# Performance work log

Hardware: AMD Instinct MI355X
Metric: run time of the kernel (lower is better)

Reference implementation:

```python
import jax, jax.numpy as jnp
import numpy as np

N = 4096          # nodes
F_IN = 1386       # txt_feat_len
NHID = 1024       # per-head hidden
NHEADS = 8
CODE = 64         # code_len
LRELU_ALPHA = 0.2
NEG_INF = -9e15


def _build_adj(x):
    # F.normalize + cosine sim, threshold 0.8, sign -> {0,1}, then symmetric D^-1/2 A D^-1/2
    norm = jnp.maximum(jnp.linalg.norm(x, axis=1, keepdims=True), 1e-12)
    xn = x / norm
    sim = xn @ xn.T                                  # (N,N)
    A = (sim >= 0.8).astype(x.dtype)                 # sign after thresholding
    rowsum = A.sum(axis=1)
    r = jnp.where(rowsum > 0, rowsum ** -0.5, 0.0)
    adj = r[:, None] * A * r[None, :]                # symmetric normalized
    return jax.lax.stop_gradient(adj)                # torch code detaches x / adj is non-diff


def _gat_head(x, W, a, adj, concat):
    # x: (N,Fin), W: (Fin,H), a: (2H,1)
    H = W.shape[1]
    Wh = x @ W                                        # (N,H)
    f1 = Wh @ a[:H]                                   # (N,1)
    f2 = Wh @ a[H:]                                   # (N,1)
    e = jax.nn.leaky_relu(f1 + f2.T, LRELU_ALPHA)     # (N,N) pairwise scores
    e = jnp.where(adj > 0, e, NEG_INF)
    att = jax.nn.softmax(e, axis=1)                   # masked softmax (dropout off: eval)
    h = att @ Wh                                      # (N,H)
    return jax.nn.elu(h) if concat else h


def setup_inputs() -> dict:
    key = jax.random.key(0)
    k = jax.random.split(key, 5)
    x = jax.random.normal(k[0], (N, F_IN), dtype=jnp.float32)
    s_in = 1.0 / np.sqrt(F_IN)
    W_att = jax.random.uniform(k[1], (NHEADS, F_IN, NHID), jnp.float32, -s_in, s_in)
    a_att = jax.random.uniform(k[2], (NHEADS, 2 * NHID, 1), jnp.float32, -0.1, 0.1)
    s_h = 1.0 / np.sqrt(NHEADS * NHID)
    W_out = jax.random.uniform(k[3], (NHEADS * NHID, CODE), jnp.float32, -s_h, s_h)
    a_out = jax.random.uniform(k[4], (2 * CODE, 1), jnp.float32, -0.1, 0.1)
    return {"x": x, "W_att": W_att, "a_att": a_att, "W_out": W_out, "a_out": a_out}


def reference(x, W_att, a_att, W_out, a_out):
    adj = _build_adj(x)
    # 8 concat heads, vmapped over the head axis
    heads = jax.vmap(lambda W, a: _gat_head(x, W, a, adj, True))(W_att, a_att)  # (8,N,NHID)
    h = jnp.transpose(heads, (1, 0, 2)).reshape(N, NHEADS * NHID)               # cat dim=1
    out = _gat_head(h, W_out, a_out, adj, False)                                # (N,CODE)
    code = jnp.tanh(1.0 * out)                                                   # alpha=1.0
    return code
```

## Files before the change

### kernel.cpp

```cpp
#include <hip/hip_runtime.h>
#include <hip/hip_bf16.h>
#include <stdint.h>
#include <math.h>


typedef __bf16 bf16x8 __attribute__((ext_vector_type(8)));
typedef float  f32x4  __attribute__((ext_vector_type(4)));
typedef int    i32x4  __attribute__((ext_vector_type(4)));
typedef unsigned short ushort8 __attribute__((ext_vector_type(8)));

#define AS1C(p) ((const __attribute__((address_space(1))) void*)(p))
#define AS3(p)  ((__attribute__((address_space(3))) void*)(p))

#define MODE_WH  0
#define MODE_F32 2

__device__ __forceinline__ float bfbits2f(unsigned short u) {
    return __uint_as_float(((unsigned)u) << 16);
}
__device__ __forceinline__ unsigned short f2bfbits(float v) {
    __hip_bfloat16 b = __float2bfloat16(v);
    return *(unsigned short*)&b;
}

__device__ __forceinline__ bool row_fast(const unsigned* __restrict__ mask,
                                         const unsigned* __restrict__ summ,
                                         int row)
{
    const uint4 s = *(const uint4*)(summ + row * 4);
    unsigned sw[4] = { s.x, s.y, s.z, s.w };
    const int wi = row >> 5;
    bool fast = (sw[wi >> 5] == (1u << (wi & 31)));
    sw[wi >> 5] = 0;
    fast = fast && !(sw[0] | sw[1] | sw[2] | sw[3]);
    return fast && (mask[row * 128 + wi] == (1u << (row & 31)));
}

template<int MODE>
__device__ __forceinline__ void gemm_body(
    __hip_bfloat16* __restrict__ As, __hip_bfloat16* __restrict__ Bs,
    int bx, int by,
    const __hip_bfloat16* __restrict__ A,
    const __hip_bfloat16* __restrict__ B,
    int lda, int ldb, int K,
    void* __restrict__ Cv, int ldc, int Nreal,
    unsigned* __restrict__ mask,
    unsigned* __restrict__ summary,
    __hip_bfloat16* __restrict__ hout)
{
    const int tid  = threadIdx.x;
    const int lane = tid & 63;
    const int wave = tid >> 6;
    const int m0   = bx * 128;
    const int n0   = by * 128;

    f32x4 acc[4][4];
#pragma unroll
    for (int i = 0; i < 4; ++i)
#pragma unroll
        for (int j = 0; j < 4; ++j)
#pragma unroll
            for (int k = 0; k < 4; ++k) acc[i][j][k] = 0.f;

    const int wm = wave >> 1, wn = wave & 1;
    const int q  = lane >> 4, ln = lane & 15;

    const int kIters = K >> 6;
    for (int kt = 0; kt < kIters; ++kt) {
        __syncthreads();
#pragma unroll
        for (int p = 0; p < 4; ++p) {
            const int t    = p * 256 + tid;
            const int half = t >> 9;
            const int tl   = t & 511;
            const int row  = tl >> 2;
            const int kb   = (tl & 3) ^ ((tl >> 3) & 3);
            const int kofs = kt * 64 + half * 32 + kb * 8;
            const __hip_bfloat16* ga = A + (long long)(m0 + row) * lda + kofs;
            const __hip_bfloat16* gb = B + (long long)(n0 + row) * ldb + kofs;
            __hip_bfloat16* sa = As + (p * 256 + wave * 64) * 8;
            __hip_bfloat16* sb = Bs + (p * 256 + wave * 64) * 8;
            __builtin_amdgcn_global_load_lds(AS1C(ga), AS3(sa), 16, 0, 0);
            __builtin_amdgcn_global_load_lds(AS1C(gb), AS3(sb), 16, 0, 0);
        }
        __syncthreads();

#pragma unroll
        for (int s = 0; s < 2; ++s) {
            bf16x8 afr[4], bfr[4];
#pragma unroll
            for (int rg = 0; rg < 4; ++rg) {
                const int r  = wm * 64 + rg * 16 + ln;
                const int sl = q ^ ((r >> 1) & 3);
                afr[rg] = *(const bf16x8*)(As + s * 4096 + r * 32 + sl * 8);
            }
#pragma unroll
            for (int cg = 0; cg < 4; ++cg) {
                const int r  = wn * 64 + cg * 16 + ln;
                const int sl = q ^ ((r >> 1) & 3);
                bfr[cg] = *(const bf16x8*)(Bs + s * 4096 + r * 32 + sl * 8);
            }
#pragma unroll
            for (int rg = 0; rg < 4; ++rg)
#pragma unroll
                for (int cg = 0; cg < 4; ++cg)
                    acc[rg][cg] = __builtin_amdgcn_mfma_f32_16x16x32_bf16(
                        afr[rg], bfr[cg], acc[rg][cg], 0, 0, 0);
        }
    }

#pragma unroll
    for (int rg = 0; rg < 4; ++rg) {
#pragma unroll
        for (int i = 0; i < 4; ++i) {
            const int row = m0 + wm * 64 + rg * 16 + q * 4 + i;
            bool fast = false;
            if (MODE == MODE_WH) fast = row_fast(mask, summary, row);
#pragma unroll
            for (int cg = 0; cg < 4; ++cg) {
                const int col = n0 + wn * 64 + cg * 16 + ln;
                const float v = acc[rg][cg][i];
                if (MODE == MODE_WH) {
                    if (fast) {
                        const float u = v > 0.f ? v : (__expf(v) - 1.f);
                        hout[(long long)row * 8192 + col] = __float2bfloat16(u);
                    } else {
                        __hip_bfloat16* C = (__hip_bfloat16*)Cv;
                        C[(long long)row * ldc + col] = __float2bfloat16(v);
                    }
                } else {
                    if (col < Nreal) {
                        float* C = (float*)Cv;
                        C[(long long)row * ldc + col] = v;
                    }
                }
            }
        }
    }
}

__device__ __forceinline__ void sim_i8_body(
    signed char* __restrict__ Aq, signed char* __restrict__ Bq,
    int bx, int by,
    const signed char* __restrict__ xq,
    const float* __restrict__ scales,
    const float* __restrict__ norms,
    unsigned* __restrict__ mask,
    unsigned* __restrict__ summary)
{
    const int tid  = threadIdx.x;
    const int lane = tid & 63;
    const int wave = tid >> 6;
    const int m0   = bx * 128;
    const int n0   = by * 128;

    i32x4 acc[4][4];
#pragma unroll
    for (int i = 0; i < 4; ++i)
#pragma unroll
        for (int j = 0; j < 4; ++j)
#pragma unroll
            for (int k = 0; k < 4; ++k) acc[i][j][k] = 0;

    const int wm = wave >> 1, wn = wave & 1;
    const int q  = lane >> 4, ln = lane & 15;

    for (int kt = 0; kt < 22; ++kt) {
        __syncthreads();
#pragma unroll
        for (int p = 0; p < 2; ++p) {
            const int t   = p * 256 + tid;
            const int row = t >> 2;
            const int kb  = (t & 3) ^ ((t >> 3) & 3);
            const signed char* ga = xq + (long long)(m0 + row) * 1408 + kt * 64 + kb * 16;
            const signed char* gb = xq + (long long)(n0 + row) * 1408 + kt * 64 + kb * 16;
            signed char* sa = Aq + (p * 256 + wave * 64) * 16;
            signed char* sb = Bq + (p * 256 + wave * 64) * 16;
            __builtin_amdgcn_global_load_lds(AS1C(ga), AS3(sa), 16, 0, 0);
            __builtin_amdgcn_global_load_lds(AS1C(gb), AS3(sb), 16, 0, 0);
        }
        __syncthreads();

        i32x4 afr[4], bfr[4];
#pragma unroll
        for (int rg = 0; rg < 4; ++rg) {
            const int r = wm * 64 + rg * 16 + ln;
            const int s = q ^ ((r >> 1) & 3);
            afr[rg] = *(const i32x4*)(Aq + r * 64 + s * 16);
        }
#pragma unroll
        for (int cg = 0; cg < 4; ++cg) {
            const int r = wn * 64 + cg * 16 + ln;
            const int s = q ^ ((r >> 1) & 3);
            bfr[cg] = *(const i32x4*)(Bq + r * 64 + s * 16);
        }
#pragma unroll
        for (int rg = 0; rg < 4; ++rg)
#pragma unroll
            for (int cg = 0; cg < 4; ++cg)
                acc[rg][cg] = __builtin_amdgcn_mfma_i32_16x16x64_i8(
                    afr[rg], bfr[cg], acc[rg][cg], 0, 0, 0);
    }

#pragma unroll
    for (int rg = 0; rg < 4; ++rg) {
#pragma unroll
        for (int i = 0; i < 4; ++i) {
            const int row = m0 + wm * 64 + rg * 16 + q * 4 + i;
            const float sr = scales[row], nr = norms[row];
#pragma unroll
            for (int cg = 0; cg < 4; ++cg) {
                const int col = n0 + wn * 64 + cg * 16 + ln;
                const float v = (float)acc[rg][cg][i] * (sr * scales[col]);
                if (v >= 0.8f * nr * norms[col]) {
                    atomicOr(&mask[row * 128 + (col >> 5)], 1u << (col & 31));
                    atomicOr(&summary[row * 4 + (col >> 10)], 1u << ((col >> 5) & 31));
                    atomicOr(&mask[col * 128 + (row >> 5)], 1u << (row & 31));
                    atomicOr(&summary[col * 4 + (row >> 10)], 1u << ((row >> 5) & 31));
                }
            }
        }
    }
}

__global__ __launch_bounds__(256)
void stage1(const float* __restrict__ x,
            const float* __restrict__ W_att,
            const float* __restrict__ W_out,
            const float* __restrict__ a_att,
            __hip_bfloat16* __restrict__ x_bf,
            signed char* __restrict__ xq,
            float* __restrict__ norms,
            float* __restrict__ scales,
            __hip_bfloat16* __restrict__ WoutT,
            float* __restrict__ wa,
            unsigned* __restrict__ mask,
            unsigned* __restrict__ summ)
{
    __shared__ float ts[32][33];
    __shared__ float red[4], redm[4], sh_s;
    const int id  = blockIdx.x;
    const int tid = threadIdx.x;

    if (id < 4096) {
        const int i = id;
        if (tid < 128) mask[i * 128 + tid] = 0;
        else if (tid < 132) summ[i * 4 + (tid - 128)] = 0;
        float ss = 0.f, am = 0.f;
        float vv[6];
#pragma unroll
        for (int k = 0; k < 6; ++k) {
            const int c = tid + k * 256;
            float v = (c < 1386) ? x[(long long)i * 1386 + c] : 0.f;
            vv[k] = v;
            if (c < 1408) x_bf[(long long)i * 1408 + c] = __float2bfloat16(v);
            ss += v * v;
            am = fmaxf(am, fabsf(v));
        }
        for (int off = 32; off; off >>= 1) {
            ss += __shfl_down(ss, off);
            am = fmaxf(am, __shfl_down(am, off));
        }
        if ((tid & 63) == 0) { red[tid >> 6] = ss; redm[tid >> 6] = am; }
        __syncthreads();
        if (tid == 0) {
            norms[i] = fmaxf(sqrtf(red[0] + red[1] + red[2] + red[3]), 1e-12f);
            const float amax = fmaxf(fmaxf(redm[0], redm[1]), fmaxf(redm[2], redm[3]));
            const float s = fmaxf(amax, 1e-30f) / 127.f;
            scales[i] = s;
            sh_s = s;
        }
        __syncthreads();
        const float inv_s = 1.f / sh_s;
#pragma unroll
        for (int k = 0; k < 6; ++k) {
            const int c = tid + k * 256;
            if (c < 1408) {
                float qv = fminf(fmaxf(rintf(vv[k] * inv_s), -127.f), 127.f);
                xq[(long long)i * 1408 + c] = (signed char)(int)qv;
            }
        }
        return;
    }
    if (id < 5120) {
        const int r  = id - 4096;
        const int k0 = (r & 255) * 32, n0 = (r >> 8) * 32;
        const int tx = tid & 31, ty = tid >> 5;
#pragma unroll
        for (int i = 0; i < 4; ++i) {
            const int k = k0 + ty + i * 8;
            const int n = n0 + tx;
            ts[ty + i * 8][tx] = (n < 64) ? W_out[(long long)k * 64 + n] : 0.f;
        }
        __syncthreads();
#pragma unroll
        for (int i = 0; i < 4; ++i) {
            const int n  = n0 + ty + i * 8;
            const int kk = k0 + tx;
            WoutT[(long long)n * 8192 + kk] = __float2bfloat16(ts[tx][ty + i * 8]);
        }
        return;
    }
    {
        const int b = id - 5120;
        const int h = b / 352, r = b % 352;
        const int wave = tid >> 6, lane = tid & 63;
        const int c = r * 4 + wave;
        float s1 = 0.f, s2 = 0.f;
        if (c < 1386) {
            const float* wr = W_att + ((long long)h * 1386 + c) * 1024;
            const float* a1 = a_att + (long long)h * 2048;
            const float* a2 = a1 + 1024;
#pragma unroll
            for (int t = 0; t < 16; ++t) {
                const int j = lane + t * 64;
                const float w = wr[j];
                s1 += w * a1[j];
                s2 += w * a2[j];
            }
        }
        for (int off = 32; off; off >>= 1) { s1 += __shfl_down(s1, off); s2 += __shfl_down(s2, off); }
        if (lane == 0 && c < 1386) {
            wa[(h * 2 + 0) * 1408 + c] = s1;
            wa[(h * 2 + 1) * 1408 + c] = s2;
        }
    }
}

__global__ __launch_bounds__(256, 2)
void stage2(const signed char* __restrict__ xq,
            const float* __restrict__ scales,
            const float* __restrict__ norms,
            unsigned* __restrict__ mask,
            unsigned* __restrict__ summ,
            const float* __restrict__ W_att,
            __hip_bfloat16* __restrict__ Wt_bf,
            const float* __restrict__ x,
            const float* __restrict__ wa,
            float2* __restrict__ f12)
{
    __shared__ __align__(16) __hip_bfloat16 As[128 * 32];
    __shared__ __align__(16) __hip_bfloat16 Bs[128 * 32];
    const int id = blockIdx.x;

    if (id < 528) {
        int t = (int)((sqrtf(8.f * id + 1.f) - 1.f) * 0.5f);
        while (t * (t + 1) / 2 > id) --t;
        while ((t + 1) * (t + 2) / 2 <= id) ++t;
        const int by = t, bx = id - t * (t + 1) / 2;
        sim_i8_body((signed char*)As, (signed char*)Bs, bx, by,
                    xq, scales, norms, mask, summ);
        return;
    }
    if (id < 11792) {
        float (*ts)[33] = (float(*)[33])As;
        const int tid = threadIdx.x;
        const int b = id - 528;
        const int h = b / 1408, r = b % 1408;
        const int kx = r % 44, ny = r / 44;
        const float* s = W_att + (long long)h * 1386 * 1024;
        __hip_bfloat16* d = Wt_bf + (long long)h * 1024 * 1408;
        const int k0 = kx * 32, n0 = ny * 32;
        const int tx = tid & 31, ty = tid >> 5;
#pragma unroll
        for (int i = 0; i < 4; ++i) {
            const int k = k0 + ty + i * 8;
            const int n = n0 + tx;
            ts[ty + i * 8][tx] = (k < 1386) ? s[(long long)k * 1024 + n] : 0.f;
        }
        __syncthreads();
#pragma unroll
        for (int i = 0; i < 4; ++i) {
            const int n  = n0 + ty + i * 8;
            const int kk = k0 + tx;
            if (kk < 1408)
                d[(long long)n * 1408 + kk] = __float2bfloat16(ts[tx][ty + i * 8]);
        }
        return;
    }
    {
        const int b    = id - 11792;
        const int wave = threadIdx.x >> 6, lane = threadIdx.x & 63;
        const int i    = b * 4 + wave;
        float s[16];
#pragma unroll
        for (int j = 0; j < 16; ++j) s[j] = 0.f;
        const float* xr = x + (long long)i * 1386;
        for (int c = lane; c < 1386; c += 64) {
            const float v = xr[c];
#pragma unroll
            for (int j = 0; j < 16; ++j) s[j] += v * wa[j * 1408 + c];
        }
#pragma unroll
        for (int j = 0; j < 16; ++j)
            for (int off = 32; off; off >>= 1) s[j] += __shfl_down(s[j], off);
        if (lane == 0) {
#pragma unroll
            for (int h = 0; h < 8; ++h)
                f12[(long long)h * 4096 + i] = make_float2(s[h * 2], s[h * 2 + 1]);
        }
    }
}

__global__ __launch_bounds__(256, 2)
void whh(const __hip_bfloat16* __restrict__ x_bf,
         const __hip_bfloat16* __restrict__ Wt_bf,
         __hip_bfloat16* __restrict__ Wh,
         __hip_bfloat16* __restrict__ hout,
         unsigned* __restrict__ mask,
         unsigned* __restrict__ summ)
{
    __shared__ __align__(16) __hip_bfloat16 As[128 * 64];
    __shared__ __align__(16) __hip_bfloat16 Bs[128 * 64];
    const int id = blockIdx.x;
    const int z  = id >> 8;
    const int r  = id & 255;
    const int bx = r & 31, by = r >> 5;
    gemm_body<MODE_WH>(As, Bs, bx, by,
                       x_bf, Wt_bf + (long long)z * 1024 * 1408,
                       1408, 1408, 1408,
                       Wh + (long long)z * 4096 * 1024, 1024, 1024,
                       mask, summ, hout + (long long)z * 1024);
}

__global__ __launch_bounds__(256, 2)
void out_gemm(const __hip_bfloat16* __restrict__ hout,
              const __hip_bfloat16* __restrict__ WoutT,
              float* __restrict__ parts)
{
    __shared__ __align__(16) __hip_bfloat16 As[128 * 64];
    __shared__ __align__(16) __hip_bfloat16 Bs[128 * 64];
    const int z = blockIdx.z;
    gemm_body<MODE_F32>(As, Bs, blockIdx.x, 0,
                        hout + z * 512, WoutT + z * 512, 8192, 8192, 512,
                        parts + (long long)z * 4096 * 64, 64, 64,
                        nullptr, nullptr, nullptr);
}

__global__ __launch_bounds__(256)
void attn_fix(const __hip_bfloat16* __restrict__ Wh,
              const float2* __restrict__ f12,
              const unsigned* __restrict__ mask,
              const unsigned* __restrict__ summary,
              __hip_bfloat16* __restrict__ hout)
{
    const int wv   = threadIdx.x >> 6;
    const int lane = threadIdx.x & 63;
    const int i    = blockIdx.x * 4 + wv;
    const int h    = blockIdx.y;
    if (row_fast(mask, summary, i)) return;

    const float2* f = f12 + (long long)h * 4096;
    const float f1 = f[i].x;
    const unsigned* mrow = mask + (long long)i * 128;
    const __hip_bfloat16* WhH = Wh + (long long)h * 4096 * 1024;
    const uint4 sm = *(const uint4*)(summary + (long long)i * 4);
    unsigned sw[4] = { sm.x, sm.y, sm.z, sm.w };
    const int cbase = lane * 16;

    float m = -INFINITY, l = 0.f;
    float acc[16];
#pragma unroll
    for (int k = 0; k < 16; ++k) acc[k] = 0.f;

#pragma unroll
    for (int s = 0; s < 4; ++s) {
        unsigned sb = sw[s];
        while (sb) {
            const int w = s * 32 + __builtin_ctz(sb);
            sb &= sb - 1;
            unsigned bits = mrow[w];
            while (bits) {
                const int j = w * 32 + __builtin_ctz(bits);
                bits &= bits - 1;
                float e = f1 + f[j].y;
                e = e > 0.f ? e : 0.2f * e;
                float wgt;
                if (e > m) {
                    const float sc = __expf(m - e);
                    l *= sc;
#pragma unroll
                    for (int k = 0; k < 16; ++k) acc[k] *= sc;
                    m = e; wgt = 1.f;
                } else {
                    wgt = __expf(e - m);
                }
                l += wgt;
                const ushort8* p = (const ushort8*)(WhH + (long long)j * 1024 + cbase);
                const ushort8 w0 = p[0], w1 = p[1];
#pragma unroll
                for (int k = 0; k < 8; ++k) acc[k]     += wgt * bfbits2f(w0[k]);
#pragma unroll
                for (int k = 0; k < 8; ++k) acc[k + 8] += wgt * bfbits2f(w1[k]);
            }
        }
    }
    const float inv = 1.f / l;
    ushort8 o0, o1;
#pragma unroll
    for (int k = 0; k < 8; ++k) {
        float v = acc[k] * inv;     v = v > 0.f ? v : (__expf(v) - 1.f); o0[k] = f2bfbits(v);
        float u = acc[k + 8] * inv; u = u > 0.f ? u : (__expf(u) - 1.f); o1[k] = f2bfbits(u);
    }
    ushort8* op = (ushort8*)(hout + (long long)i * 8192 + (long long)h * 1024 + cbase);
    op[0] = o0; op[1] = o1;
}

__global__ __launch_bounds__(256)
void out_finish(const float* __restrict__ parts,
                const float* __restrict__ a_out,
                float* __restrict__ Cout,
                float* __restrict__ f1o,
                float* __restrict__ f2o,
                const unsigned* __restrict__ mask,
                const unsigned* __restrict__ summ,
                float* __restrict__ out)
{
    const int wv = threadIdx.x >> 6;
    const int c  = threadIdx.x & 63;
    const int i  = blockIdx.x * 4 + wv;
    float v = 0.f;
#pragma unroll
    for (int z = 0; z < 16; ++z) v += parts[(long long)z * 4096 * 64 + (long long)i * 64 + c];
    Cout[(long long)i * 64 + c] = v;
    float s1 = v * a_out[c];
    float s2 = v * a_out[64 + c];
    for (int off = 32; off; off >>= 1) { s1 += __shfl_down(s1, off); s2 += __shfl_down(s2, off); }
    if (c == 0) { f1o[i] = s1; f2o[i] = s2; }
    if (row_fast(mask, summ, i))
        out[(long long)i * 64 + c] = tanhf(v);
}

__global__ __launch_bounds__(256)
void attn_out_fix(const float* __restrict__ Cout,
                  const float* __restrict__ f1o,
                  const float* __restrict__ f2o,
                  const unsigned* __restrict__ mask,
                  const unsigned* __restrict__ summary,
                  float* __restrict__ out)
{
    const int wv = threadIdx.x >> 6;
    const int c  = threadIdx.x & 63;
    const int i  = blockIdx.x * 4 + wv;
    if (row_fast(mask, summary, i)) return;
    const float f1 = f1o[i];
    const unsigned* mrow = mask + (long long)i * 128;
    const uint4 sm = *(const uint4*)(summary + (long long)i * 4);
    unsigned sw[4] = { sm.x, sm.y, sm.z, sm.w };
    float m = -INFINITY, l = 0.f, acc = 0.f;
#pragma unroll
    for (int s = 0; s < 4; ++s) {
        unsigned sb = sw[s];
        while (sb) {
            const int w = s * 32 + __builtin_ctz(sb);
            sb &= sb - 1;
            unsigned bits = mrow[w];
            while (bits) {
                const int j = w * 32 + __builtin_ctz(bits);
                bits &= bits - 1;
                float e = f1 + f2o[j];
                e = e > 0.f ? e : 0.2f * e;
                float wgt;
                if (e > m) { const float sc = __expf(m - e); l *= sc; acc *= sc; m = e; wgt = 1.f; }
                else       { wgt = __expf(e - m); }
                l += wgt;
                acc += wgt * Cout[(long long)j * 64 + c];
            }
        }
    }
    out[(long long)i * 64 + c] = tanhf(acc / l);
}

extern "C" void kernel_launch(void* const* d_in, const int* in_sizes, int n_in,
                              void* d_out, int out_size, void* d_ws, size_t ws_size,
                              hipStream_t stream)
{
    (void)in_sizes; (void)n_in; (void)out_size;
    const float* x     = (const float*)d_in[0];
    const float* W_att = (const float*)d_in[1];
    const float* a_att = (const float*)d_in[2];
    const float* W_out = (const float*)d_in[3];
    const float* a_out = (const float*)d_in[4];
    float* out = (float*)d_out;

    char* ws = (char*)d_ws;
    size_t off = 0;
    auto alloc = [&](size_t bytes) -> void* {
        void* p = ws + off;
        off += (bytes + 255) & ~(size_t)255;
        return p;
    };

    __hip_bfloat16* x_bf  = (__hip_bfloat16*)alloc(4096LL * 1408 * 2);
    signed char*    xq    = (signed char*)alloc(4096LL * 1408);
    __hip_bfloat16* Wt_bf = (__hip_bfloat16*)alloc(8LL * 1024 * 1408 * 2);
    __hip_bfloat16* WoutT = (__hip_bfloat16*)alloc(128LL * 8192 * 2);
    float*          norms = (float*)alloc(4096 * 4);
    float*          scales= (float*)alloc(4096 * 4);
    unsigned*       mask  = (unsigned*)alloc(4096LL * 128 * 4);
    unsigned*       summ  = (unsigned*)alloc(4096LL * 4 * 4);
    float*          wa    = (float*)alloc(16LL * 1408 * 4);
    float2*         f12   = (float2*)alloc(8LL * 4096 * 8);
    float*          parts = (float*)alloc(16LL * 4096 * 64 * 4);
    float*          Cout  = (float*)alloc(4096LL * 64 * 4);
    float*          f1o   = (float*)alloc(4096 * 4);
    float*          f2o   = (float*)alloc(4096 * 4);
    __hip_bfloat16* Wh    = (__hip_bfloat16*)alloc(8LL * 4096 * 1024 * 2);
    __hip_bfloat16* hout  = (__hip_bfloat16*)alloc(8LL * 4096 * 1024 * 2);
    if (off > ws_size) return;

    stage1<<<7936, 256, 0, stream>>>(x, W_att, W_out, a_att,
                                     x_bf, xq, norms, scales, WoutT, wa,
                                     mask, summ);

    stage2<<<12816, 256, 0, stream>>>(xq, scales, norms, mask, summ,
                                      W_att, Wt_bf, x, wa, f12);

    whh<<<2048, 256, 0, stream>>>(x_bf, Wt_bf, Wh, hout, mask, summ);

    attn_fix<<<dim3(1024, 8), 256, 0, stream>>>(Wh, f12, mask, summ, hout);

    out_gemm<<<dim3(32, 1, 16), 256, 0, stream>>>(hout, WoutT, parts);

    out_finish<<<1024, 256, 0, stream>>>(parts, a_out, Cout, f1o, f2o,
                                         mask, summ, out);
    attn_out_fix<<<1024, 256, 0, stream>>>(Cout, f1o, f2o, mask, summ, out);
}
```

Measured before the change: 296.2 us.

## Merge Wh GEMM with similarity pass into one launch and move W_att transpose earlier

Moves the W_att bf16 transpose into stage1 and fuses the per-head Wh GEMM, the int8 similarity/mask build and the f12 projection into a single 'mega' kernel, so the Wh GEMM no longer waits on the adjacency mask. Because the mask is no longer ready when the GEMM epilogue runs, the epilogue now always writes both raw Wh and the ELU'd hout, and attn_fix overwrites the non-fast rows later. The output GEMM split-K goes from 16 to 8 partitions, which halves the partial buffer and the reduction. The cost is extra hout writes for every row and a longer K loop per out_gemm block.

```diff
diff --git a/kernel.cpp b/kernel.cpp
--- a/kernel.cpp
+++ b/kernel.cpp
@@ -44,8 +44,6 @@
     const __hip_bfloat16* __restrict__ B,
     int lda, int ldb, int K,
     void* __restrict__ Cv, int ldc, int Nreal,
-    unsigned* __restrict__ mask,
-    unsigned* __restrict__ summary,
     __hip_bfloat16* __restrict__ hout)
 {
     const int tid  = threadIdx.x;
@@ -114,20 +112,15 @@
 #pragma unroll
         for (int i = 0; i < 4; ++i) {
             const int row = m0 + wm * 64 + rg * 16 + q * 4 + i;
-            bool fast = false;
-            if (MODE == MODE_WH) fast = row_fast(mask, summary, row);
 #pragma unroll
             for (int cg = 0; cg < 4; ++cg) {
                 const int col = n0 + wn * 64 + cg * 16 + ln;
                 const float v = acc[rg][cg][i];
                 if (MODE == MODE_WH) {
-                    if (fast) {
-                        const float u = v > 0.f ? v : (__expf(v) - 1.f);
-                        hout[(long long)row * 8192 + col] = __float2bfloat16(u);
-                    } else {
-                        __hip_bfloat16* C = (__hip_bfloat16*)Cv;
-                        C[(long long)row * ldc + col] = __float2bfloat16(v);
-                    }
+                    __hip_bfloat16* C = (__hip_bfloat16*)Cv;
+                    C[(long long)row * ldc + col] = __float2bfloat16(v);
+                    const float u = v > 0.f ? v : (__expf(v) - 1.f);
+                    hout[(long long)row * 8192 + col] = __float2bfloat16(u);
                 } else {
                     if (col < Nreal) {
                         float* C = (float*)Cv;
@@ -233,6 +226,7 @@
             float* __restrict__ norms,
             float* __restrict__ scales,
             __hip_bfloat16* __restrict__ WoutT,
+            __hip_bfloat16* __restrict__ Wt_bf,
             float* __restrict__ wa,
             unsigned* __restrict__ mask,
             unsigned* __restrict__ summ)
@@ -282,27 +276,42 @@
         }
         return;
     }
-    if (id < 5120) {
-        const int r  = id - 4096;
-        const int k0 = (r & 255) * 32, n0 = (r >> 8) * 32;
+    if (id < 16384) {
+        const float* s; __hip_bfloat16* d;
+        int K, N, Kpad, k0, n0;
+        if (id < 5120) {
+            const int r = id - 4096;
+            s = W_out; d = WoutT;
+            K = 8192; N = 64; Kpad = 8192;
+            k0 = (r & 255) * 32; n0 = (r >> 8) * 32;
+        } else {
+            const int b = id - 5120;
+            const int h = b / 1408, r = b % 1408;
+            const int kx = r % 44, ny = r / 44;
+            s = W_att + (long long)h * 1386 * 1024;
+            d = Wt_bf + (long long)h * 1024 * 1408;
+            K = 1386; N = 1024; Kpad = 1408;
+            k0 = kx * 32; n0 = ny * 32;
+        }
         const int tx = tid & 31, ty = tid >> 5;
 #pragma unroll
         for (int i = 0; i < 4; ++i) {
             const int k = k0 + ty + i * 8;
             const int n = n0 + tx;
-            ts[ty + i * 8][tx] = (n < 64) ? W_out[(long long)k * 64 + n] : 0.f;
+            ts[ty + i * 8][tx] = (k < K && n < N) ? s[(long long)k * N + n] : 0.f;
         }
         __syncthreads();
 #pragma unroll
         for (int i = 0; i < 4; ++i) {
             const int n  = n0 + ty + i * 8;
             const int kk = k0 + tx;
-            WoutT[(long long)n * 8192 + kk] = __float2bfloat16(ts[tx][ty + i * 8]);
+            if (kk < Kpad)
+                d[(long long)n * Kpad + kk] = __float2bfloat16(ts[tx][ty + i * 8]);
         }
         return;
     }
     {
-        const int b = id - 5120;
+        const int b = id - 16384;
         const int h = b / 352, r = b % 352;
         const int wave = tid >> 6, lane = tid & 63;
         const int c = r * 4 + wave;
@@ -328,58 +337,46 @@
 }
 
 __global__ __launch_bounds__(256, 2)
-void stage2(const signed char* __restrict__ xq,
-            const float* __restrict__ scales,
-            const float* __restrict__ norms,
-            unsigned* __restrict__ mask,
-            unsigned* __restrict__ summ,
-            const float* __restrict__ W_att,
-            __hip_bfloat16* __restrict__ Wt_bf,
-            const float* __restrict__ x,
-            const float* __restrict__ wa,
-            float2* __restrict__ f12)
-{
-    __shared__ __align__(16) __hip_bfloat16 As[128 * 32];
-    __shared__ __align__(16) __hip_bfloat16 Bs[128 * 32];
+void mega(const __hip_bfloat16* __restrict__ x_bf,
+          const __hip_bfloat16* __restrict__ Wt_bf,
+          __hip_bfloat16* __restrict__ Wh,
+          __hip_bfloat16* __restrict__ hout,
+          const signed char* __restrict__ xq,
+          const float* __restrict__ scales,
+          const float* __restrict__ norms,
+          unsigned* __restrict__ mask,
+          unsigned* __restrict__ summ,
+          const float* __restrict__ x,
+          const float* __restrict__ wa,
+          float2* __restrict__ f12)
+{
+    __shared__ __align__(16) __hip_bfloat16 As[128 * 64];
+    __shared__ __align__(16) __hip_bfloat16 Bs[128 * 64];
     const int id = blockIdx.x;
 
-    if (id < 528) {
-        int t = (int)((sqrtf(8.f * id + 1.f) - 1.f) * 0.5f);
-        while (t * (t + 1) / 2 > id) --t;
-        while ((t + 1) * (t + 2) / 2 <= id) ++t;
-        const int by = t, bx = id - t * (t + 1) / 2;
+    if (id < 2048) {
+        const int z  = id >> 8;
+        const int r  = id & 255;
+        const int bx = r & 31, by = r >> 5;
+        gemm_body<MODE_WH>(As, Bs, bx, by,
+                           x_bf, Wt_bf + (long long)z * 1024 * 1408,
+                           1408, 1408, 1408,
+                           Wh + (long long)z * 4096 * 1024, 1024, 1024,
+                           hout + (long long)z * 1024);
+        return;
+    }
+    if (id < 2576) {
+        const int s2 = id - 2048;
+        int t = (int)((sqrtf(8.f * s2 + 1.f) - 1.f) * 0.5f);
+        while (t * (t + 1) / 2 > s2) --t;
+        while ((t + 1) * (t + 2) / 2 <= s2) ++t;
+        const int by = t, bx = s2 - t * (t + 1) / 2;
         sim_i8_body((signed char*)As, (signed char*)Bs, bx, by,
                     xq, scales, norms, mask, summ);
         return;
     }
-    if (id < 11792) {
-        float (*ts)[33] = (float(*)[33])As;
-        const int tid = threadIdx.x;
-        const int b = id - 528;
-        const int h = b / 1408, r = b % 1408;
-        const int kx = r % 44, ny = r / 44;
-        const float* s = W_att + (long long)h * 1386 * 1024;
-        __hip_bfloat16* d = Wt_bf + (long long)h * 1024 * 1408;
-        const int k0 = kx * 32, n0 = ny * 32;
-        const int tx = tid & 31, ty = tid >> 5;
-#pragma unroll
-        for (int i = 0; i < 4; ++i) {
-            const int k = k0 + ty + i * 8;
-            const int n = n0 + tx;
-            ts[ty + i * 8][tx] = (k < 1386) ? s[(long long)k * 1024 + n] : 0.f;
-        }
-        __syncthreads();
-#pragma unroll
-        for (int i = 0; i < 4; ++i) {
-            const int n  = n0 + ty + i * 8;
-            const int kk = k0 + tx;
-            if (kk < 1408)
-                d[(long long)n * 1408 + kk] = __float2bfloat16(ts[tx][ty + i * 8]);
-        }
-        return;
-    }
     {
-        const int b    = id - 11792;
+        const int b    = id - 2576;
         const int wave = threadIdx.x >> 6, lane = threadIdx.x & 63;
         const int i    = b * 4 + wave;
         float s[16];
@@ -403,27 +400,6 @@
 }
 
 __global__ __launch_bounds__(256, 2)
-void whh(const __hip_bfloat16* __restrict__ x_bf,
-         const __hip_bfloat16* __restrict__ Wt_bf,
-         __hip_bfloat16* __restrict__ Wh,
-         __hip_bfloat16* __restrict__ hout,
-         unsigned* __restrict__ mask,
-         unsigned* __restrict__ summ)
-{
-    __shared__ __align__(16) __hip_bfloat16 As[128 * 64];
-    __shared__ __align__(16) __hip_bfloat16 Bs[128 * 64];
-    const int id = blockIdx.x;
-    const int z  = id >> 8;
-    const int r  = id & 255;
-    const int bx = r & 31, by = r >> 5;
-    gemm_body<MODE_WH>(As, Bs, bx, by,
-                       x_bf, Wt_bf + (long long)z * 1024 * 1408,
-                       1408, 1408, 1408,
-                       Wh + (long long)z * 4096 * 1024, 1024, 1024,
-                       mask, summ, hout + (long long)z * 1024);
-}
-
-__global__ __launch_bounds__(256, 2)
 void out_gemm(const __hip_bfloat16* __restrict__ hout,
               const __hip_bfloat16* __restrict__ WoutT,
               float* __restrict__ parts)
@@ -432,9 +408,9 @@
     __shared__ __align__(16) __hip_bfloat16 Bs[128 * 64];
     const int z = blockIdx.z;
     gemm_body<MODE_F32>(As, Bs, blockIdx.x, 0,
-                        hout + z * 512, WoutT + z * 512, 8192, 8192, 512,
+                        hout + z * 1024, WoutT + z * 1024, 8192, 8192, 1024,
                         parts + (long long)z * 4096 * 64, 64, 64,
-                        nullptr, nullptr, nullptr);
+                        nullptr);
 }
 
 __global__ __launch_bounds__(256)
@@ -521,7 +497,7 @@
     const int i  = blockIdx.x * 4 + wv;
     float v = 0.f;
 #pragma unroll
-    for (int z = 0; z < 16; ++z) v += parts[(long long)z * 4096 * 64 + (long long)i * 64 + c];
+    for (int z = 0; z < 8; ++z) v += parts[(long long)z * 4096 * 64 + (long long)i * 64 + c];
     Cout[(long long)i * 64 + c] = v;
     float s1 = v * a_out[c];
     float s2 = v * a_out[64 + c];
@@ -601,7 +577,7 @@
     unsigned*       summ  = (unsigned*)alloc(4096LL * 4 * 4);
     float*          wa    = (float*)alloc(16LL * 1408 * 4);
     float2*         f12   = (float2*)alloc(8LL * 4096 * 8);
-    float*          parts = (float*)alloc(16LL * 4096 * 64 * 4);
+    float*          parts = (float*)alloc(8LL * 4096 * 64 * 4);
     float*          Cout  = (float*)alloc(4096LL * 64 * 4);
     float*          f1o   = (float*)alloc(4096 * 4);
     float*          f2o   = (float*)alloc(4096 * 4);
@@ -609,18 +585,17 @@
     __hip_bfloat16* hout  = (__hip_bfloat16*)alloc(8LL * 4096 * 1024 * 2);
     if (off > ws_size) return;
 
-    stage1<<<7936, 256, 0, stream>>>(x, W_att, W_out, a_att,
-                                     x_bf, xq, norms, scales, WoutT, wa,
-                                     mask, summ);
-
-    stage2<<<12816, 256, 0, stream>>>(xq, scales, norms, mask, summ,
-                                      W_att, Wt_bf, x, wa, f12);
-
-    whh<<<2048, 256, 0, stream>>>(x_bf, Wt_bf, Wh, hout, mask, summ);
+    stage1<<<19200, 256, 0, stream>>>(x, W_att, W_out, a_att,
+                                      x_bf, xq, norms, scales, WoutT, Wt_bf,
+                                      wa, mask, summ);
+
+    mega<<<3600, 256, 0, stream>>>(x_bf, Wt_bf, Wh, hout,
+                                   xq, scales, norms, mask, summ,
+                                   x, wa, f12);
 
     attn_fix<<<dim3(1024, 8), 256, 0, stream>>>(Wh, f12, mask, summ, hout);
 
-    out_gemm<<<dim3(32, 1, 16), 256, 0, stream>>>(hout, WoutT, parts);
+    out_gemm<<<dim3(32, 1, 8), 256, 0, stream>>>(hout, WoutT, parts);
 
     out_finish<<<1024, 256, 0, stream>>>(parts, a_out, Cout, f1o, f2o,
                                          mask, summ, out);
```

Result: no change. 301.2 us (+1.7%).
